# Kernel optimization log

Hardware: AMD Instinct MI355X
Metric: run time of the kernel (lower is better)

The kernel has to match this reference:

```python
import jax, jax.numpy as jnp
import numpy as np

N, E, D, ED, B, MAXN, GF, MIX = 1024, 2048, 256, 128, 16, 64, 38, 10
EPS = 1e-5


def setup_inputs() -> dict:
    key = jax.random.key(0)
    ks = jax.random.split(key, 16)

    def w(k, shape, fan_in, scale=1.0):
        return jax.random.normal(k, shape, jnp.float32) * (scale / np.sqrt(fan_in))

    return {
        "x": jax.random.normal(ks[0], (N, GF), jnp.float32),
        "edge_attr": jax.random.uniform(ks[1], (E, 4), jnp.float32),
        "edge_index": jax.random.randint(ks[2], (2, E), 0, N),
        "lin_w": w(ks[3], (D, GF), GF), "lin_b": jnp.zeros((D,), jnp.float32),
        "bn_g": jnp.ones((D,), jnp.float32), "bn_b": jnp.zeros((D,), jnp.float32),
        "nn_w1": w(ks[4], (ED, 4), 4), "nn_b1": jnp.zeros((ED,), jnp.float32),
        "nn_w2": w(ks[5], (D * D, ED), ED, 0.1), "nn_b2": jnp.zeros((D * D,), jnp.float32),
        "root_w": w(ks[6], (D, D), D), "conv_b": jnp.zeros((D,), jnp.float32),
        "gru_wih": w(ks[7], (3 * D, D), D), "gru_whh": w(ks[8], (3 * D, D), D),
        "gru_bih": jnp.zeros((3 * D,), jnp.float32), "gru_bhh": jnp.zeros((3 * D,), jnp.float32),
        "mlp_w1": w(ks[9], (MIX, D, D), D), "mlp_b1": jnp.zeros((MIX, D), jnp.float32),
        "mlp_w2": w(ks[10], (MIX, D, D), D), "mlp_b2": jnp.zeros((MIX, D), jnp.float32),
        "mlp_w3": w(ks[11], (MIX, 1, D), D), "mlp_b3": jnp.zeros((MIX, 1), jnp.float32),
    }


def reference(x, edge_attr, edge_index, lin_w, lin_b, bn_g, bn_b, nn_w1, nn_b1,
              nn_w2, nn_b2, root_w, conv_b, gru_wih, gru_whh, gru_bih, gru_bhh,
              mlp_w1, mlp_b1, mlp_w2, mlp_b2, mlp_w3, mlp_b3):
    src, dst = edge_index[0], edge_index[1]

    # input embed + BatchNorm1d (training-mode batch statistics)
    y = x @ lin_w.T + lin_b
    mean, var = y.mean(0), y.var(0)
    xh = (y - mean) / jnp.sqrt(var + EPS) * bn_g + bn_b

    # edge-conditioned NNConv weights: per-edge [D, D] matrix from edge MLP
    hidden = jax.nn.sigmoid(edge_attr @ nn_w1.T + nn_b1)          # [E, ED]
    We = (hidden @ nn_w2.T + nn_b2).reshape(E, D, D)               # [E, D, D]

    cnt = jax.ops.segment_sum(jnp.ones((E,), jnp.float32), dst, num_segments=N)
    denom = jnp.maximum(cnt, 1.0)[:, None]                         # mean aggregation

    def conv(xn):
        msg = jnp.einsum('ed,edf->ef', xn[src], We)                # per-edge matmul
        agg = jax.ops.segment_sum(msg, dst, num_segments=N) / denom
        return agg + xn @ root_w.T + conv_b                        # NNConv root + bias

    def gru(xn, h):                                                # torch GRU cell math
        gi = xn @ gru_wih.T + gru_bih
        gh = h @ gru_whh.T + gru_bhh
        ir, iz, inn = jnp.split(gi, 3, -1)
        hr, hz, hn = jnp.split(gh, 3, -1)
        r = jax.nn.sigmoid(ir + hr)
        z = jax.nn.sigmoid(iz + hz)
        n = jnp.tanh(inn + r * hn)
        return (1.0 - z) * n + z * h

    h = xh
    xc = xh
    for _ in range(3):
        m = jax.nn.relu(conv(xc))
        h = gru(m, h)
        xc = h

    vert = xc.reshape(B, MAXN, D)                                  # [B, MAX_N, D]
    h1 = jax.nn.relu(jnp.einsum('bnd,mkd->mbnk', vert, mlp_w1) + mlp_b1[:, None, None, :])
    h2 = jax.nn.relu(jnp.einsum('mbnk,mjk->mbnj', h1, mlp_w2) + mlp_b2[:, None, None, :])
    mix = jnp.einsum('mbnk,mjk->mbnj', h2, mlp_w3) + mlp_b3[:, None, None, :]  # [MIX,B,MAX_N,1]

    # bootstrap_compute, eval mode: mean over mixtures, unbiased std
    mu = mix.mean(0)
    std = jnp.sqrt(mix.var(0, ddof=1) + EPS)
    return mu, std
```

## Files before the change

### kernel.cpp

```cpp
#include <hip/hip_runtime.h>
#include <hip/hip_bf16.h>
#include <math.h>

typedef _Float16 f16;
typedef _Float16 f16x8 __attribute__((ext_vector_type(8)));
typedef _Float16 f16x4 __attribute__((ext_vector_type(4)));
typedef _Float16 f16x2 __attribute__((ext_vector_type(2)));
typedef _Float16 half2v __attribute__((ext_vector_type(2)));
typedef float    f32x4 __attribute__((ext_vector_type(4)));

#define NN 1024
#define EE 2048
#define DD 256
#define EDH 128

typedef const __attribute__((address_space(1))) void gas_t;
typedef __attribute__((address_space(3))) void las_t;
#define GLOAD16(g, l) __builtin_amdgcn_global_load_lds((gas_t*)(g), (las_t*)(l), 16, 0, 0)

#if __has_builtin(__builtin_amdgcn_fdot2)
#define DOT2(a, b, c) __builtin_amdgcn_fdot2((a), (b), (c), false)
#else
#define DOT2(a, b, c) ((float)(a)[0]*(float)(b)[0] + (float)(a)[1]*(float)(b)[1] + (c))
#endif


__global__ __launch_bounds__(256) void k_embed_hidden(const float* __restrict__ x,
    const float* __restrict__ lw, const float* __restrict__ lb,
    const float* __restrict__ ea, const float* __restrict__ w1, const float* __restrict__ b1,
    float* __restrict__ y, float* __restrict__ colsum, float* __restrict__ colsq,
    f16* __restrict__ h16e) {
  int bid = blockIdx.x, t = threadIdx.x;
  if (bid < 256) {
    int n0 = bid*4;
    __shared__ float xr[4][38];
    if (t < 152) ((float*)xr)[t] = x[n0*38 + t];
    __syncthreads();
    float b0 = lb[t];
    float s0 = b0, s1 = b0, s2 = b0, s3 = b0;
    const float* w = lw + t*38;
    #pragma unroll
    for (int d = 0; d < 38; d++) {
      float wd = w[d];
      s0 += xr[0][d]*wd; s1 += xr[1][d]*wd; s2 += xr[2][d]*wd; s3 += xr[3][d]*wd;
    }
    y[(n0+0)*DD + t] = s0; y[(n0+1)*DD + t] = s1;
    y[(n0+2)*DD + t] = s2; y[(n0+3)*DD + t] = s3;
    atomicAdd(&colsum[t], s0+s1+s2+s3);
    atomicAdd(&colsq[t], s0*s0+s1*s1+s2*s2+s3*s3);
  } else {
    int e = (bid - 256)*2 + (t >> 7);
    int k = t & 127;
    const float* a = ea + e*4;
    const float* w = w1 + k*4;
    float s = b1[k] + a[0]*w[0] + a[1]*w[1] + a[2]*w[2] + a[3]*w[3];
    h16e[e*EDH + k] = (f16)(1.f / (1.f + expf(-s)));
  }
}

__global__ __launch_bounds__(256) void k_bnapply(const float* __restrict__ y,
    const float* __restrict__ colsum, const float* __restrict__ colsq,
    const float* __restrict__ g, const float* __restrict__ b,
    float* __restrict__ xh, f16* __restrict__ xc16) {
  int i = blockIdx.x*256 + threadIdx.x;
  int c = i & 255;
  float mean = colsum[c] * (1.f/1024.f);
  float var  = colsq[c] * (1.f/1024.f) - mean*mean;
  float sc = g[c] / sqrtf(var + 1e-5f);
  float sh = b[c] - mean*sc;
  float v = y[i]*sc + sh;
  xh[i] = v;
  xc16[i] = (f16)v;
}


__global__ __launch_bounds__(1024) void k_csr(const int* __restrict__ ei,
    int* __restrict__ cntAll, int* __restrict__ offAll, float* __restrict__ denomB,
    unsigned* __restrict__ rec, int* __restrict__ srcD) {
  __shared__ int cntD[1024], cntS[1024], curD[1024], curS[1024], sc[1024];
  int t = threadIdx.x;
  cntD[t] = 0; cntS[t] = 0;
  __syncthreads();
  #pragma unroll
  for (int r = 0; r < 2; r++) {
    int e = r*1024 + t;
    atomicAdd(&cntD[ei[EE + e]], 1);
    atomicAdd(&cntS[ei[e]], 1);
  }
  __syncthreads();
  int cD = cntD[t], cS = cntS[t];
  sc[t] = cD; __syncthreads();
  for (int o = 1; o < 1024; o <<= 1) {
    int v = (t >= o) ? sc[t - o] : 0;
    __syncthreads(); sc[t] += v; __syncthreads();
  }
  int exD = sc[t] - cD;
  curD[t] = exD;
  cntAll[t] = cD; offAll[t] = exD;
  denomB[t] = (float)(cD > 1 ? cD : 1);
  __syncthreads();
  sc[t] = cS; __syncthreads();
  for (int o = 1; o < 1024; o <<= 1) {
    int v = (t >= o) ? sc[t - o] : 0;
    __syncthreads(); sc[t] += v; __syncthreads();
  }
  int exS = sc[t] - cS;
  curS[t] = exS;
  offAll[1024 + t] = exS;
  __syncthreads();
  #pragma unroll
  for (int r = 0; r < 2; r++) {
    int e = r*1024 + t;
    int d = ei[EE + e], s2 = ei[e];
    int pD = atomicAdd(&curD[d], 1);
    int pS = atomicAdd(&curS[s2], 1);
    rec[pS] = (unsigned)e | ((unsigned)s2 << 11) | ((unsigned)pD << 21);
    srcD[pD] = s2;
  }
}


__global__ __launch_bounds__(256) void k_w2tr(const float* __restrict__ w2, f16* __restrict__ BTb) {
  __shared__ f16 ls[128][130];
  int f = blockIdx.x, dh = blockIdx.y, t = threadIdx.x;
  int dl = t >> 1, kh = (t & 1) * 64;
  const float* src = w2 + ((size_t)(dh*128 + dl)*256 + f)*128 + kh;
  #pragma unroll
  for (int i = 0; i < 16; i++) {
    f32x4 v = *(const f32x4*)(src + i*4);
    f16x2 a = {(f16)v[0], (f16)v[1]};
    f16x2 b = {(f16)v[2], (f16)v[3]};
    *(f16x2*)(&ls[dl][kh + i*4])     = a;
    *(f16x2*)(&ls[dl][kh + i*4 + 2]) = b;
  }
  __syncthreads();
  int k = t >> 1, dh2 = (t & 1) * 64;
  f16* dst = BTb + ((size_t)f*128 + k)*256 + dh*128 + dh2;
  #pragma unroll
  for (int g = 0; g < 8; g++) {
    f16x8 pk;
    #pragma unroll
    for (int q = 0; q < 8; q++) pk[q] = ls[dh2 + g*8 + q][k];
    *(f16x8*)(dst + g*8) = pk;
  }
}


__global__ __launch_bounds__(256) void k_prepw(const float* __restrict__ s0, f16* __restrict__ d0,
    const float* __restrict__ s1, f16* __restrict__ d1,
    const float* __restrict__ s2, f16* __restrict__ d2,
    const float* __restrict__ s3, f16* __restrict__ d3,
    const float* __restrict__ rw, const float* __restrict__ nb2, f16* __restrict__ Bside) {
  int bid = blockIdx.x, t = threadIdx.x;
  if (bid < 1664) {
    const float* src; f16* dst; int i;
    if      (bid < 192)  { src = s0; dst = d0; i = bid*256 + t; }
    else if (bid < 384)  { src = s1; dst = d1; i = (bid-192)*256 + t; }
    else if (bid < 1024) { src = s2; dst = d2; i = (bid-384)*256 + t; }
    else                 { src = s3; dst = d3; i = (bid-1024)*256 + t; }
    f32x4 v = ((const f32x4*)src)[i];
    f16x4 r; r[0]=(f16)v[0]; r[1]=(f16)v[1]; r[2]=(f16)v[2]; r[3]=(f16)v[3];
    ((f16x4*)dst)[i] = r;
  } else if (bid < 1728) {
    int i = (bid - 1664)*256 + t;
    f32x4 v = *(const f32x4*)(rw + (size_t)i*4);
    f16x4 r; r[0]=(f16)v[0]; r[1]=(f16)v[1]; r[2]=(f16)v[2]; r[3]=(f16)v[3];
    *(f16x4*)(Bside + 65536 + (size_t)i*4) = r;
  } else {
    __shared__ float ls[64][65];
    int fb = bid - 1728;
    for (int db = 0; db < 4; db++) {
      int r = t >> 2, cs = (t & 3) * 16;
      const float* s = nb2 + (size_t)(db*64 + r)*256 + fb*64 + cs;
      #pragma unroll
      for (int i = 0; i < 16; i += 4) {
        f32x4 v = *(const f32x4*)(s + i);
        ls[r][cs+i] = v[0]; ls[r][cs+i+1] = v[1]; ls[r][cs+i+2] = v[2]; ls[r][cs+i+3] = v[3];
      }
      __syncthreads();
      int fl = t >> 2, ds2 = (t & 3) * 16;
      f16x8 p0, p1;
      #pragma unroll
      for (int q = 0; q < 8; q++) { p0[q] = (f16)ls[ds2+q][fl]; p1[q] = (f16)ls[ds2+8+q][fl]; }
      f16* d = Bside + (size_t)(fb*64 + fl)*256 + db*64 + ds2;
      *(f16x8*)(d)     = p0;
      *(f16x8*)(d + 8) = p1;
      __syncthreads();
    }
  }
}


__global__ __launch_bounds__(256) void k_fgemm(const f16* __restrict__ A,
    const f16* __restrict__ BTb, const f16* __restrict__ Bside, const f16* __restrict__ Wbh,
    const f16* __restrict__ h16e, const int* __restrict__ offAll,
    const unsigned* __restrict__ rec, float* __restrict__ T2R,
    float* __restrict__ G2, float* __restrict__ msgbuf) {
  __shared__ __align__(16) f16 lds[17408];
  int raw = blockIdx.x;
  int pmod = raw & 7, q = raw >> 3;
  int m = q & 7, pg = q >> 3;
  int p = pg*8 + pmod;
  if (p >= 266) return;
  int m0 = m*128;
  int t = threadIdx.x;
  int lane = t & 63, wv = t >> 6, wm = wv >> 1, wn = wv & 1;
  int lr = lane & 15, lg = lane >> 4;
  const f16* Bbase = (p < 256) ? (BTb + (size_t)p*32768)
                   : (p < 260) ? (Bside + (size_t)(p-256)*32768)
                               : (Wbh + (size_t)(p-260)*32768);
  int e0 = wv*1024 + lane*8;
  int r0 = e0 >> 5, c0 = e0 & 31;
  int e1 = e0 + 512;
  int r1 = e1 >> 5, c1 = e1 & 31;
  const f16* Ag0 = A + (size_t)(m0 + r0)*256 + c0;
  const f16* Ag1 = A + (size_t)(m0 + r1)*256 + c1;
  const f16* Bg0 = Bbase + (size_t)r0*256 + c0;
  const f16* Bg1 = Bbase + (size_t)r1*256 + c1;
  f16* As = lds;
  f16* Bs = lds + 8192;
  f16* Al0 = As + wv*1024; f16* Al1 = Al0 + 512;
  f16* Bl0 = Bs + wv*1024; f16* Bl1 = Bl0 + 512;
  f32x4 acc[4][4] = {};
  for (int k0 = 0; k0 < 256; k0 += 64) {
    __syncthreads();
    GLOAD16(Ag0 + k0,      Al0);
    GLOAD16(Ag1 + k0,      Al1);
    GLOAD16(Ag0 + k0 + 32, Al0 + 4096);
    GLOAD16(Ag1 + k0 + 32, Al1 + 4096);
    GLOAD16(Bg0 + k0,      Bl0);
    GLOAD16(Bg1 + k0,      Bl1);
    GLOAD16(Bg0 + k0 + 32, Bl0 + 4096);
    GLOAD16(Bg1 + k0 + 32, Bl1 + 4096);
    __syncthreads();
    #pragma unroll
    for (int P = 0; P < 2; P++) {
      f16x8 af[4], bf[4];
      #pragma unroll
      for (int i = 0; i < 4; i++)
        af[i] = *(const f16x8*)(&As[P*4096 + (wm*64 + i*16 + lr)*32 + lg*8]);
      #pragma unroll
      for (int j = 0; j < 4; j++)
        bf[j] = *(const f16x8*)(&Bs[P*4096 + (wn*64 + j*16 + lr)*32 + lg*8]);
      #pragma unroll
      for (int i = 0; i < 4; i++)
        #pragma unroll
        for (int j = 0; j < 4; j++)
          acc[i][j] = __builtin_amdgcn_mfma_f32_16x16x32_f16(af[i], bf[j], acc[i][j], 0, 0, 0);
    }
  }
  if (p >= 260) {
    int c0o = (p - 260)*128;
    #pragma unroll
    for (int i = 0; i < 4; i++)
      #pragma unroll
      for (int j = 0; j < 4; j++)
        #pragma unroll
        for (int v = 0; v < 4; v++)
          G2[(size_t)(m0 + wm*64 + i*16 + lg*4 + v)*768 + c0o + wn*64 + j*16 + lr] = acc[i][j][v];
    return;
  }
  if (p >= 256) {
    int c0o = (p - 256)*128;
    #pragma unroll
    for (int i = 0; i < 4; i++)
      #pragma unroll
      for (int j = 0; j < 4; j++)
        #pragma unroll
        for (int v = 0; v < 4; v++)
          T2R[(size_t)(m0 + wm*64 + i*16 + lg*4 + v)*512 + c0o + wn*64 + j*16 + lr] = acc[i][j][v];
    return;
  }
  __syncthreads();
  #pragma unroll
  for (int i = 0; i < 4; i++)
    #pragma unroll
    for (int j = 0; j < 4; j++)
      #pragma unroll
      for (int v = 0; v < 4; v++)
        lds[(wm*64 + i*16 + lg*4 + v)*136 + wn*64 + j*16 + lr] = (f16)acc[i][j][v];
  __syncthreads();
  int eS = offAll[1024 + m0];
  int eE = (m0 < 896) ? offAll[1024 + m0 + 128] : EE;
  for (int idx = eS + t; idx < eE; idx += 256) {
    unsigned u = rec[idx];
    int e = u & 2047, src = (u >> 11) & 1023, pos = (int)(u >> 21);
    int r = src - m0;
    const f16* hp = h16e + (size_t)e*EDH;
    float sp0 = 0.f, sp1 = 0.f, sp2 = 0.f, sp3 = 0.f;
    #pragma unroll
    for (int i = 0; i < 4; i++) {
      #pragma unroll
      for (int c = 0; c < 4; c++) {
        int blk = i*4 + c;
        f16x8 hv = *(const f16x8*)(hp + blk*8);
        f16x8 tv = *(const f16x8*)(&lds[r*136 + blk*8]);
        union { f16x8 v8; half2v pr[4]; } hu, tu;
        hu.v8 = hv; tu.v8 = tv;
        float s = (c == 0) ? sp0 : (c == 1) ? sp1 : (c == 2) ? sp2 : sp3;
        #pragma unroll
        for (int qd = 0; qd < 4; qd++) s = DOT2(hu.pr[qd], tu.pr[qd], s);
        if      (c == 0) sp0 = s;
        else if (c == 1) sp1 = s;
        else if (c == 2) sp2 = s;
        else             sp3 = s;
      }
    }
    msgbuf[(size_t)pos*256 + p] = (sp0 + sp1) + (sp2 + sp3);
  }
}


__global__ __launch_bounds__(256) void k_fin(const float* __restrict__ msgbuf,
    const int* __restrict__ cntAll, const int* __restrict__ offAll,
    const float* __restrict__ denomB, const float* __restrict__ T2R,
    const int* __restrict__ srcD, const float* __restrict__ cb, f16* __restrict__ Am) {
  int n = blockIdx.x, t = threadIdx.x;
  int deg = cntAll[n], o = offAll[n];
  float s = 0.f;
  for (int j = 0; j < deg; j++)
    s += msgbuf[(size_t)(o+j)*256 + t] + T2R[(size_t)srcD[o+j]*512 + t];
  float m = s / denomB[n] + T2R[(size_t)n*512 + 256 + t] + cb[t];
  Am[(size_t)n*256 + t] = (f16)fmaxf(m, 0.f);
}


__global__ __launch_bounds__(256) void k_gemm64(const f16* __restrict__ A,
    const f16* __restrict__ BT, float* __restrict__ C) {
  __shared__ __align__(16) f16 As[64*40];
  __shared__ __align__(16) f16 Bs[64*40];
  int t = threadIdx.x;
  int m0 = blockIdx.x*64, n0 = blockIdx.y*64;
  int lane = t & 63, wv = t >> 6, wm = wv >> 1, wn = wv & 1;
  int lr = lane & 15, lk = (lane >> 4) * 8;
  int arow = t >> 2, aseg = (t & 3) * 8;
  f32x4 acc[2][2] = {};
  for (int k0 = 0; k0 < 256; k0 += 32) {
    __syncthreads();
    *(f16x8*)(&As[arow*40 + aseg]) = *(const f16x8*)(A + (size_t)(m0 + arow)*256 + k0 + aseg);
    *(f16x8*)(&Bs[arow*40 + aseg]) = *(const f16x8*)(BT + (size_t)(n0 + arow)*256 + k0 + aseg);
    __syncthreads();
    f16x8 af[2], bf[2];
    #pragma unroll
    for (int i = 0; i < 2; i++) af[i] = *(const f16x8*)(&As[(wm*32 + i*16 + lr)*40 + lk]);
    #pragma unroll
    for (int j = 0; j < 2; j++) bf[j] = *(const f16x8*)(&Bs[(wn*32 + j*16 + lr)*40 + lk]);
    #pragma unroll
    for (int i = 0; i < 2; i++)
      #pragma unroll
      for (int j = 0; j < 2; j++)
        acc[i][j] = __builtin_amdgcn_mfma_f32_16x16x32_f16(af[i], bf[j], acc[i][j], 0, 0, 0);
  }
  #pragma unroll
  for (int i = 0; i < 2; i++)
    #pragma unroll
    for (int j = 0; j < 2; j++)
      #pragma unroll
      for (int v = 0; v < 4; v++) {
        int r = m0 + wm*32 + i*16 + (lane >> 4)*4 + v;
        int cc = n0 + wn*32 + j*16 + lr;
        C[(size_t)r*768 + cc] = acc[i][j][v];
      }
}


template<int MODE>
__global__ __launch_bounds__(256) void k_gemm_sm(const f16* __restrict__ A,
    const f16* __restrict__ BT, float* __restrict__ C, f16* __restrict__ Ch,
    const float* __restrict__ bias, int K, int lda, int ldb, int N,
    int bsA, int bsB, int bsC, int bsBias) {
  __shared__ __align__(16) f16 As[64*40];
  __shared__ __align__(16) f16 Bs[128*40];
  int t = threadIdx.x;
  int m0 = blockIdx.x*64, n0 = blockIdx.y*128, z = blockIdx.z;
  A  += (size_t)z * bsA;
  BT += (size_t)z * bsB;
  if constexpr (MODE == 1) C += (size_t)z * bsC;
  else { Ch += (size_t)z * bsC; bias += (size_t)z * bsBias; }
  int lane = t & 63, wv = t >> 6, wm = wv >> 1, wn = wv & 1;
  int lr = lane & 15, lk = (lane >> 4) * 8;
  int arow = t >> 2, aseg = (t & 3) * 8;
  f32x4 acc[2][4] = {};
  for (int k0 = 0; k0 < K; k0 += 32) {
    __syncthreads();
    *(f16x8*)(&As[arow*40 + aseg]) = *(const f16x8*)(A + (size_t)(m0 + arow)*lda + k0 + aseg);
    *(f16x8*)(&Bs[arow*40 + aseg]) = *(const f16x8*)(BT + (size_t)(n0 + arow)*ldb + k0 + aseg);
    *(f16x8*)(&Bs[(64+arow)*40 + aseg]) = *(const f16x8*)(BT + (size_t)(n0 + 64 + arow)*ldb + k0 + aseg);
    __syncthreads();
    f16x8 af[2], bf[4];
    #pragma unroll
    for (int i = 0; i < 2; i++) af[i] = *(const f16x8*)(&As[(wm*32 + i*16 + lr)*40 + lk]);
    #pragma unroll
    for (int j = 0; j < 4; j++) bf[j] = *(const f16x8*)(&Bs[(wn*64 + j*16 + lr)*40 + lk]);
    #pragma unroll
    for (int i = 0; i < 2; i++)
      #pragma unroll
      for (int j = 0; j < 4; j++)
        acc[i][j] = __builtin_amdgcn_mfma_f32_16x16x32_f16(af[i], bf[j], acc[i][j], 0, 0, 0);
  }
  #pragma unroll
  for (int i = 0; i < 2; i++)
    #pragma unroll
    for (int j = 0; j < 4; j++)
      #pragma unroll
      for (int v = 0; v < 4; v++) {
        int r = m0 + wm*32 + i*16 + (lane >> 4)*4 + v;
        int cc = n0 + wn*64 + j*16 + lr;
        float val = acc[i][j][v];
        if constexpr (MODE == 1) {
          C[(size_t)r*N + cc] = val;
        } else {
          val += bias[cc];
          val = fmaxf(val, 0.f);
          Ch[(size_t)r*N + cc] = (f16)val;
        }
      }
}


__global__ __launch_bounds__(256) void k_gate(const float* __restrict__ gi,
    const float* __restrict__ gh, const float* __restrict__ bih, const float* __restrict__ bhh,
    const float* __restrict__ hOld, float* __restrict__ hNew, f16* __restrict__ xc16) {
  int i = blockIdx.x*256 + threadIdx.x;
  int row = i >> 8, c = i & 255;
  const float* gir = gi + (size_t)row*768;
  const float* ghr = gh + (size_t)row*768;
  float ir  = gir[c]     + bih[c],     hr = ghr[c]     + bhh[c];
  float iz  = gir[256+c] + bih[256+c], hz = ghr[256+c] + bhh[256+c];
  float inn = gir[512+c] + bih[512+c], hn = ghr[512+c] + bhh[512+c];
  float r  = 1.f / (1.f + expf(-(ir + hr)));
  float zz = 1.f / (1.f + expf(-(iz + hz)));
  float nn = tanhf(inn + r*hn);
  float hv = (1.f - zz)*nn + zz*hOld[i];
  hNew[i] = hv;
  xc16[i] = (f16)hv;
}


__global__ __launch_bounds__(256) void k_mix(const f16* __restrict__ h2,
    const float* __restrict__ w3, const float* __restrict__ b3, float* __restrict__ mix) {
  int b = blockIdx.x, t = threadIdx.x;
  int wv = t >> 6, lane = t & 63;
  int rid = b*4 + wv;
  int m = rid >> 10, row = rid & 1023;
  const f16* hr = h2 + (size_t)(m*1024 + row)*DD;
  const float* w = w3 + m*DD;
  float s = 0.f;
  #pragma unroll
  for (int q = 0; q < 4; q++) { int d = lane + q*64; s += (float)hr[d] * w[d]; }
  #pragma unroll
  for (int o = 32; o; o >>= 1) s += __shfl_down(s, o, 64);
  if (lane == 0) mix[m*1024 + row] = s + b3[m];
}

__global__ __launch_bounds__(256) void k_out(const float* __restrict__ mix, float* __restrict__ out) {
  int i = blockIdx.x*256 + threadIdx.x;
  float v[10]; float mu = 0.f;
  #pragma unroll
  for (int m = 0; m < 10; m++) { v[m] = mix[m*1024 + i]; mu += v[m]; }
  mu *= 0.1f;
  float var = 0.f;
  #pragma unroll
  for (int m = 0; m < 10; m++) { float d = v[m] - mu; var += d*d; }
  var *= (1.f/9.f);
  out[i] = mu;
  out[1024 + i] = sqrtf(var + 1e-5f);
}


extern "C" void kernel_launch(void* const* d_in, const int* in_sizes, int n_in,
                              void* d_out, int out_size, void* d_ws, size_t ws_size,
                              hipStream_t stream) {
  const float* x         = (const float*)d_in[0];
  const float* edge_attr = (const float*)d_in[1];
  const int*   edge_idx  = (const int*)  d_in[2];
  const float* lin_w     = (const float*)d_in[3];
  const float* lin_b     = (const float*)d_in[4];
  const float* bn_g      = (const float*)d_in[5];
  const float* bn_b      = (const float*)d_in[6];
  const float* nn_w1     = (const float*)d_in[7];
  const float* nn_b1     = (const float*)d_in[8];
  const float* nn_w2     = (const float*)d_in[9];
  const float* nn_b2     = (const float*)d_in[10];
  const float* root_w    = (const float*)d_in[11];
  const float* conv_b    = (const float*)d_in[12];
  const float* gru_wih   = (const float*)d_in[13];
  const float* gru_whh   = (const float*)d_in[14];
  const float* gru_bih   = (const float*)d_in[15];
  const float* gru_bhh   = (const float*)d_in[16];
  const float* mlp_w1    = (const float*)d_in[17];
  const float* mlp_b1    = (const float*)d_in[18];
  const float* mlp_w2    = (const float*)d_in[19];
  const float* mlp_b2    = (const float*)d_in[20];
  const float* mlp_w3    = (const float*)d_in[21];
  const float* mlp_b3    = (const float*)d_in[22];
  float* out = (float*)d_out;

  char* w = (char*)d_ws;
  size_t o = 0;
  auto nxt = [&](size_t b) -> size_t { size_t r = o; o += (b + 255) & ~(size_t)255; return r; };
  float* y      = (float*)(w + nxt(1048576));
  float* colsum = (float*)(w + nxt(1024));
  float* colsq  = (float*)(w + nxt(1024));
  float* xh     = (float*)(w + nxt(1048576));
  float* h      = (float*)(w + nxt(1048576));
  f16*   xc16   = (f16*)  (w + nxt(524288));
  f16*   h16e   = (f16*)  (w + nxt(524288));
  int*   cntAll = (int*)  (w + nxt(4096));
  int*   offAll = (int*)  (w + nxt(8192));
  float* denomB = (float*)(w + nxt(4096));
  unsigned* rec = (unsigned*)(w + nxt(8192));
  int*   srcD   = (int*)  (w + nxt(8192));
  f16*   BTb    = (f16*)  (w + nxt((size_t)32768*256*2));
  f16*   Bside  = (f16*)  (w + nxt((size_t)512*256*2));
  float* T2R    = (float*)(w + nxt((size_t)1024*512*4));
  float* msgbuf = (float*)(w + nxt((size_t)EE*256*4));
  f16*   Am     = (f16*)  (w + nxt(524288));
  float* G      = (float*)(w + nxt((size_t)2*1024*768*4));
  f16*   Wb     = (f16*)  (w + nxt(786432));
  f16*   w1T    = (f16*)  (w + nxt(1310720));
  f16*   w2T    = (f16*)  (w + nxt(1310720));
  f16*   h1     = (f16*)  (w + nxt(5242880));
  f16*   h2     = (f16*)  (w + nxt(5242880));
  float* mixb   = (float*)(w + nxt(40960));
  if (o > ws_size) return;

  hipMemsetAsync(colsum, 0, 2048, stream);

  k_embed_hidden<<<1280, 256, 0, stream>>>(x, lin_w, lin_b, edge_attr, nn_w1, nn_b1,
                                           y, colsum, colsq, h16e);
  k_bnapply<<<1024, 256, 0, stream>>>(y, colsum, colsq, bn_g, bn_b, xh, xc16);
  k_csr  <<<1, 1024, 0, stream>>>(edge_idx, cntAll, offAll, denomB, rec, srcD);
  k_w2tr <<<dim3(256, 2), 256, 0, stream>>>(nn_w2, BTb);
  k_prepw<<<1732, 256, 0, stream>>>(gru_wih, Wb, gru_whh, Wb + 196608,
                                    mlp_w1, w1T, mlp_w2, w2T, root_w, nn_b2, Bside);

  for (int it = 0; it < 3; it++) {
    const float* hOld = (it == 0) ? xh : h;
    k_fgemm<<<2176, 256, 0, stream>>>(xc16, BTb, Bside, Wb + 196608, h16e, offAll,
                                      rec, T2R, G + 786432, msgbuf);
    k_fin  <<<1024, 256, 0, stream>>>(msgbuf, cntAll, offAll, denomB, T2R, srcD, conv_b, Am);
    k_gemm64<<<dim3(16, 12), 256, 0, stream>>>(Am, Wb, G);
    k_gate<<<1024, 256, 0, stream>>>(G, G + 786432, gru_bih, gru_bhh, hOld, h, xc16);
  }

  k_gemm_sm<3><<<dim3(16, 2, 10), 256, 0, stream>>>(xc16, w1T, nullptr, h1, mlp_b1,
      256, 256, 256, 256, 0, 65536, 262144, 256);
  k_gemm_sm<3><<<dim3(16, 2, 10), 256, 0, stream>>>(h1, w2T, nullptr, h2, mlp_b2,
      256, 256, 256, 256, 262144, 65536, 262144, 256);
  k_mix<<<2560, 256, 0, stream>>>(h2, mlp_w3, mlp_b3, mixb);
  k_out<<<4, 256, 0, stream>>>(mixb, out);
}
```

Measured before the change: 252.4 us.

## Halve fgemm row tile, swizzle LDS staging, split edge dot across thread pairs

The fused GEMM kernel now uses 64-row M tiles instead of 128, which doubles the grid and shrinks LDS and accumulator registers per block, aiming for more occupancy and parallelism. The staged f16 result tile in LDS uses an XOR swizzle in place of padding to avoid bank conflicts. The per-edge 128-wide dot product is split between two threads and combined with a shuffle, so more threads work on each block's edge range. The cost is that B tiles are loaded twice as often in total, because each B tile is now reused across only 64 rows.

```diff
diff --git a/kernel.cpp b/kernel.cpp
--- a/kernel.cpp
+++ b/kernel.cpp
@@ -196,38 +196,37 @@
     const f16* __restrict__ h16e, const int* __restrict__ offAll,
     const unsigned* __restrict__ rec, float* __restrict__ T2R,
     float* __restrict__ G2, float* __restrict__ msgbuf) {
-  __shared__ __align__(16) f16 lds[17408];
+  __shared__ __align__(16) f16 lds[12288];
   int raw = blockIdx.x;
   int pmod = raw & 7, q = raw >> 3;
-  int m = q & 7, pg = q >> 3;
+  int m = q & 15, pg = q >> 4;
   int p = pg*8 + pmod;
   if (p >= 266) return;
-  int m0 = m*128;
+  int m0 = m*64;
   int t = threadIdx.x;
   int lane = t & 63, wv = t >> 6, wm = wv >> 1, wn = wv & 1;
   int lr = lane & 15, lg = lane >> 4;
   const f16* Bbase = (p < 256) ? (BTb + (size_t)p*32768)
                    : (p < 260) ? (Bside + (size_t)(p-256)*32768)
                                : (Wbh + (size_t)(p-260)*32768);
+  int ea = wv*512 + lane*8;
+  int ra = ea >> 5, ca = ea & 31;
+  const f16* AgA = A + (size_t)(m0 + ra)*256 + ca;
   int e0 = wv*1024 + lane*8;
   int r0 = e0 >> 5, c0 = e0 & 31;
   int e1 = e0 + 512;
   int r1 = e1 >> 5, c1 = e1 & 31;
-  const f16* Ag0 = A + (size_t)(m0 + r0)*256 + c0;
-  const f16* Ag1 = A + (size_t)(m0 + r1)*256 + c1;
   const f16* Bg0 = Bbase + (size_t)r0*256 + c0;
   const f16* Bg1 = Bbase + (size_t)r1*256 + c1;
   f16* As = lds;
-  f16* Bs = lds + 8192;
-  f16* Al0 = As + wv*1024; f16* Al1 = Al0 + 512;
+  f16* Bs = lds + 4096;
+  f16* AlA = As + wv*512;
   f16* Bl0 = Bs + wv*1024; f16* Bl1 = Bl0 + 512;
-  f32x4 acc[4][4] = {};
+  f32x4 acc[2][4] = {};
   for (int k0 = 0; k0 < 256; k0 += 64) {
     __syncthreads();
-    GLOAD16(Ag0 + k0,      Al0);
-    GLOAD16(Ag1 + k0,      Al1);
-    GLOAD16(Ag0 + k0 + 32, Al0 + 4096);
-    GLOAD16(Ag1 + k0 + 32, Al1 + 4096);
+    GLOAD16(AgA + k0,      AlA);
+    GLOAD16(AgA + k0 + 32, AlA + 2048);
     GLOAD16(Bg0 + k0,      Bl0);
     GLOAD16(Bg1 + k0,      Bl1);
     GLOAD16(Bg0 + k0 + 32, Bl0 + 4096);
@@ -235,15 +234,15 @@
     __syncthreads();
     #pragma unroll
     for (int P = 0; P < 2; P++) {
-      f16x8 af[4], bf[4];
-      #pragma unroll
-      for (int i = 0; i < 4; i++)
-        af[i] = *(const f16x8*)(&As[P*4096 + (wm*64 + i*16 + lr)*32 + lg*8]);
+      f16x8 af[2], bf[4];
+      #pragma unroll
+      for (int i = 0; i < 2; i++)
+        af[i] = *(const f16x8*)(&As[P*2048 + (wm*32 + i*16 + lr)*32 + lg*8]);
       #pragma unroll
       for (int j = 0; j < 4; j++)
         bf[j] = *(const f16x8*)(&Bs[P*4096 + (wn*64 + j*16 + lr)*32 + lg*8]);
       #pragma unroll
-      for (int i = 0; i < 4; i++)
+      for (int i = 0; i < 2; i++)
         #pragma unroll
         for (int j = 0; j < 4; j++)
           acc[i][j] = __builtin_amdgcn_mfma_f32_16x16x32_f16(af[i], bf[j], acc[i][j], 0, 0, 0);
@@ -252,61 +251,61 @@
   if (p >= 260) {
     int c0o = (p - 260)*128;
     #pragma unroll
-    for (int i = 0; i < 4; i++)
+    for (int i = 0; i < 2; i++)
       #pragma unroll
       for (int j = 0; j < 4; j++)
         #pragma unroll
         for (int v = 0; v < 4; v++)
-          G2[(size_t)(m0 + wm*64 + i*16 + lg*4 + v)*768 + c0o + wn*64 + j*16 + lr] = acc[i][j][v];
+          G2[(size_t)(m0 + wm*32 + i*16 + lg*4 + v)*768 + c0o + wn*64 + j*16 + lr] = acc[i][j][v];
     return;
   }
   if (p >= 256) {
     int c0o = (p - 256)*128;
     #pragma unroll
-    for (int i = 0; i < 4; i++)
+    for (int i = 0; i < 2; i++)
       #pragma unroll
       for (int j = 0; j < 4; j++)
         #pragma unroll
         for (int v = 0; v < 4; v++)
-          T2R[(size_t)(m0 + wm*64 + i*16 + lg*4 + v)*512 + c0o + wn*64 + j*16 + lr] = acc[i][j][v];
+          T2R[(size_t)(m0 + wm*32 + i*16 + lg*4 + v)*512 + c0o + wn*64 + j*16 + lr] = acc[i][j][v];
     return;
   }
   __syncthreads();
   #pragma unroll
-  for (int i = 0; i < 4; i++)
+  for (int i = 0; i < 2; i++)
     #pragma unroll
     for (int j = 0; j < 4; j++)
       #pragma unroll
-      for (int v = 0; v < 4; v++)
-        lds[(wm*64 + i*16 + lg*4 + v)*136 + wn*64 + j*16 + lr] = (f16)acc[i][j][v];
+      for (int v = 0; v < 4; v++) {
+        int r = wm*32 + i*16 + lg*4 + v;
+        int c = wn*64 + j*16 + lr;
+        lds[r*128 + (((c >> 3) ^ (r & 7)) << 3) + (c & 7)] = (f16)acc[i][j][v];
+      }
   __syncthreads();
   int eS = offAll[1024 + m0];
-  int eE = (m0 < 896) ? offAll[1024 + m0 + 128] : EE;
-  for (int idx = eS + t; idx < eE; idx += 256) {
+  int eE = (m0 + 64 < 1024) ? offAll[1024 + m0 + 64] : EE;
+  int g = t & 1, es = t >> 1;
+  for (int idx = eS + es; idx < eE; idx += 128) {
     unsigned u = rec[idx];
     int e = u & 2047, src = (u >> 11) & 1023, pos = (int)(u >> 21);
     int r = src - m0;
-    const f16* hp = h16e + (size_t)e*EDH;
-    float sp0 = 0.f, sp1 = 0.f, sp2 = 0.f, sp3 = 0.f;
-    #pragma unroll
-    for (int i = 0; i < 4; i++) {
-      #pragma unroll
-      for (int c = 0; c < 4; c++) {
-        int blk = i*4 + c;
-        f16x8 hv = *(const f16x8*)(hp + blk*8);
-        f16x8 tv = *(const f16x8*)(&lds[r*136 + blk*8]);
-        union { f16x8 v8; half2v pr[4]; } hu, tu;
-        hu.v8 = hv; tu.v8 = tv;
-        float s = (c == 0) ? sp0 : (c == 1) ? sp1 : (c == 2) ? sp2 : sp3;
-        #pragma unroll
-        for (int qd = 0; qd < 4; qd++) s = DOT2(hu.pr[qd], tu.pr[qd], s);
-        if      (c == 0) sp0 = s;
-        else if (c == 1) sp1 = s;
-        else if (c == 2) sp2 = s;
-        else             sp3 = s;
-      }
+    const f16* hp = h16e + (size_t)e*EDH + g*64;
+    float s0 = 0.f, s1 = 0.f;
+    #pragma unroll
+    for (int i = 0; i < 8; i++) {
+      int blk = g*8 + i;
+      f16x8 hv = *(const f16x8*)(hp + i*8);
+      f16x8 tv = *(const f16x8*)(&lds[r*128 + ((blk ^ (r & 7)) << 3)]);
+      union { f16x8 v8; half2v pr[4]; } hu, tu;
+      hu.v8 = hv; tu.v8 = tv;
+      float sx = (i & 1) ? s1 : s0;
+      #pragma unroll
+      for (int qd = 0; qd < 4; qd++) sx = DOT2(hu.pr[qd], tu.pr[qd], sx);
+      if (i & 1) s1 = sx; else s0 = sx;
     }
-    msgbuf[(size_t)pos*256 + p] = (sp0 + sp1) + (sp2 + sp3);
+    float s = s0 + s1;
+    s += __shfl_xor(s, 1, 64);
+    if (g == 0) msgbuf[(size_t)pos*256 + p] = s;
   }
 }
 
@@ -537,7 +536,7 @@
 
   for (int it = 0; it < 3; it++) {
     const float* hOld = (it == 0) ? xh : h;
-    k_fgemm<<<2176, 256, 0, stream>>>(xc16, BTb, Bside, Wb + 196608, h16e, offAll,
+    k_fgemm<<<4352, 256, 0, stream>>>(xc16, BTb, Bside, Wb + 196608, h16e, offAll,
                                       rec, T2R, G + 786432, msgbuf);
     k_fin  <<<1024, 256, 0, stream>>>(msgbuf, cntAll, offAll, denomB, T2R, srcD, conv_b, Am);
     k_gemm64<<<dim3(16, 12), 256, 0, stream>>>(Am, Wb, G);
```

After: 238.4 us. -5.5%, faster.
